# Performance work log

Hardware: AMD Instinct MI355X
Metric: run time of the kernel (lower is better)

The kernel has to match this reference:

```python
import jax, jax.numpy as jnp
import numpy as np

# --- constants from init_kwargs / module defaults ---
H, W, C = 720, 1280, 2
T_EVT, T_PROP = 10, 10
T_TOTAL = T_EVT + T_PROP          # 20 temporal steps (10 event + 10 propagation)
TAU, THR0 = 10.0, 1.0             # LIF time constant, base threshold
ALPHA, TARGET_RATE = 0.1, 0.1     # PENT adaptation
THR_MIN, THR_MAX = 0.1, 10.0
N_EVENTS = 4_000_000


def setup_inputs() -> dict:
    key = jax.random.key(0)
    k1, k2, k3, k4 = jax.random.split(key, 4)
    x = jax.random.randint(k1, (N_EVENTS,), 0, W, dtype=jnp.int32)
    y = jax.random.randint(k2, (N_EVENTS,), 0, H, dtype=jnp.int32)
    p = jax.random.randint(k3, (N_EVENTS,), 0, 2, dtype=jnp.int32)
    t = jax.random.uniform(k4, (N_EVENTS,), dtype=jnp.float32)
    return {"x": x, "y": y, "p": p, "t": t}


def _build_buffer(x, y, p, t):
    # TemporalBuffer.forward: bin events into first T_EVT steps, rest are zeros.
    tmin, tmax = t.min(), t.max()
    denom = jnp.where(tmax > tmin, tmax - tmin, jnp.float32(1.0))
    t_norm = jnp.where(tmax > tmin, (t - tmin) / denom * (T_EVT - 1e-6), 0.0)
    t_idx = jnp.clip(t_norm.astype(jnp.int32), 0, T_EVT - 1)
    xi = jnp.clip(x, 0, W - 1)
    yi = jnp.clip(y, 0, H - 1)
    c_idx = p  # p in {0,1} -> channel index directly (p.min() >= 0 branch)
    buf = jnp.zeros((T_TOTAL, C, H, W), jnp.float32)
    return buf.at[t_idx, c_idx, yi, xi].add(1.0)


def reference(x, y, p, t):
    buffer = _build_buffer(x, y, p, t)  # (T, C, H, W)
    decay = jnp.float32(np.exp(-1.0 / TAU))

    def step(carry, frame):
        mem, thr = carry
        # LIFBuffer: decay + accumulate
        mem = mem * decay + frame
        spk = (mem >= thr).astype(jnp.float32)
        mem = mem - spk * thr  # soft ('subtract') reset
        # AdaptiveThreshold (PENT): homeostatic rate-based adaptation
        rate = spk.mean()
        thr = jnp.clip(thr + ALPHA * (rate - TARGET_RATE), THR_MIN, THR_MAX)
        return (mem, thr), spk

    mem0 = jnp.zeros((C, H, W), jnp.float32)
    (_, _), spikes = jax.lax.scan(step, (mem0, jnp.float32(THR0)), buffer)
    return spikes  # (T, C, H, W) binary spike activity maps
```

## Files before the change

### kernel.cpp

```cpp
#include <hip/hip_runtime.h>
#include <cstddef>

#define HH 720
#define WW 1280
#define FRAME 1843200
#define FRAME4 460800
#define T_EVT 10
#define T_TOTAL 20
#define ARRIVE64 (1ULL << 32)

#define ONBLK 256
#define ONTHR 1024
#define ONWPB 16
#define ONT (ONBLK * ONTHR)

#define SBLK 1024
#define STHR 256
#define SWPB 4
#define PIXB 1800
#define NGROUP4 450
#define HIST_W 9000
#define RBLK 512
#define RTHR 1024
#define OTHR 512
#define NBUCKET 1024

#define MAT_OFF   0u
#define CS_OFF    (512u * 1024u * 4u)
#define SB_OFF    (CS_OFF + 4096u)
#define KEY_OFF   (SB_OFF + 8192u)
#define SEG_OFF(n) (KEY_OFF + 4u * (unsigned)(n))
#define WS_NEED(n) ((size_t)SEG_OFF(n) + 2ull * (size_t)(n) + 256ull)

__device__ unsigned g_minkey;
__device__ unsigned g_maxkey;
__device__ unsigned long long g_grp[T_TOTAL][16][16];
__device__ unsigned long long g_top[T_TOTAL][16];
__device__ unsigned g_rel[T_TOTAL][32];
__device__ unsigned long long g_n1[T_TOTAL][64][16];
__device__ unsigned long long g_n2[T_TOTAL][4][16];
__device__ unsigned long long g_n3[T_TOTAL][16];
__device__ unsigned g_relg[T_TOTAL][64][32];

__device__ __forceinline__ unsigned f2key(float f) {
    unsigned b = __float_as_uint(f);
    return b ^ ((unsigned)(((int)b) >> 31) | 0x80000000u);
}
__device__ __forceinline__ float key2f(unsigned k) {
    unsigned b = (k & 0x80000000u) ? (k ^ 0x80000000u) : ~k;
    return __uint_as_float(b);
}

__device__ __forceinline__ int event_bin_t(float tv, float tmin, float tmax) {
#pragma clang fp contract(off)
    float tn;
    if (tmax > tmin) tn = (tv - tmin) / (tmax - tmin) * (float)(10.0 - 1e-6);
    else tn = 0.0f;
    int ti = (int)tn;
    return ti < 0 ? 0 : (ti > T_EVT - 1 ? T_EVT - 1 : ti);
}
__device__ __forceinline__ int event_pixel(int xi, int yi, int ci) {
    xi = xi < 0 ? 0 : (xi > WW - 1 ? WW - 1 : xi);
    yi = yi < 0 ? 0 : (yi > HH - 1 ? HH - 1 : yi);
    return ci * (HH * WW) + yi * WW + xi;
}

__global__ void init_kernel() {
    const int gtid = blockIdx.x * blockDim.x + threadIdx.x;
    const int gs = gridDim.x * blockDim.x;
    if (gtid == 0) { g_minkey = 0xFFFFFFFFu; g_maxkey = 0u; }
    unsigned long long* a = &g_grp[0][0][0];
    for (int i = gtid; i < T_TOTAL * 16 * 16; i += gs) a[i] = 0ull;
    unsigned long long* b = &g_top[0][0];
    for (int i = gtid; i < T_TOTAL * 16; i += gs) b[i] = 0ull;
    unsigned* c = &g_rel[0][0];
    for (int i = gtid; i < T_TOTAL * 32; i += gs) c[i] = 0u;
    unsigned long long* d = &g_n1[0][0][0];
    for (int i = gtid; i < T_TOTAL * 64 * 16; i += gs) d[i] = 0ull;
    unsigned long long* e = &g_n2[0][0][0];
    for (int i = gtid; i < T_TOTAL * 4 * 16; i += gs) e[i] = 0ull;
    unsigned long long* f = &g_n3[0][0];
    for (int i = gtid; i < T_TOTAL * 16; i += gs) f[i] = 0ull;
    unsigned* g = &g_relg[0][0][0];
    for (int i = gtid; i < T_TOTAL * 64 * 32; i += gs) g[i] = 0u;
}

__device__ __forceinline__ void minmax_body(const float* __restrict__ t, int n,
                                            int gtid, int gstride) {
    unsigned mn = 0xFFFFFFFFu, mx = 0u;
    const int n4 = n >> 2;
    const float4* t4 = (const float4*)t;
    for (int i = gtid; i < n4; i += gstride) {
        float4 tv = t4[i];
        unsigned k0 = f2key(tv.x), k1 = f2key(tv.y);
        unsigned k2 = f2key(tv.z), k3 = f2key(tv.w);
        unsigned a = k0 < k1 ? k0 : k1, b = k2 < k3 ? k2 : k3;
        unsigned c = a < b ? a : b;
        mn = mn < c ? mn : c;
        a = k0 > k1 ? k0 : k1; b = k2 > k3 ? k2 : k3;
        c = a > b ? a : b;
        mx = mx > c ? mx : c;
    }
    for (int i = (n4 << 2) + gtid; i < n; i += gstride) {
        unsigned k = f2key(t[i]);
        mn = mn < k ? mn : k;
        mx = mx > k ? mx : k;
    }
    for (int off = 32; off > 0; off >>= 1) {
        unsigned omn = (unsigned)__shfl_down((int)mn, off, 64);
        unsigned omx = (unsigned)__shfl_down((int)mx, off, 64);
        mn = mn < omn ? mn : omn;
        mx = mx > omx ? mx : omx;
    }
    __shared__ unsigned smn[16], smx[16];
    int lane = threadIdx.x & 63, wv = threadIdx.x >> 6;
    if (lane == 0) { smn[wv] = mn; smx[wv] = mx; }
    __syncthreads();
    if (threadIdx.x == 0) {
        int nw = blockDim.x >> 6;
        for (int i = 1; i < nw; ++i) {
            mn = mn < smn[i] ? mn : smn[i];
            mx = mx > smx[i] ? mx : smx[i];
        }
        atomicMin(&g_minkey, mn);
        atomicMax(&g_maxkey, mx);
    }
}

__global__ void minmax_zero_kernel(const float* __restrict__ t, int n,
                                   uint4* __restrict__ hist16v) {
    const int gtid = blockIdx.x * blockDim.x + threadIdx.x;
    const int gstride = gridDim.x * blockDim.x;
    const uint4 z = make_uint4(0u, 0u, 0u, 0u);
    const int nz = T_EVT * FRAME / 8;
    for (int i = gtid; i < nz; i += gstride) hist16v[i] = z;
    minmax_body(t, n, gtid, gstride);
}

__global__ __launch_bounds__(RTHR) void passA_kernel(
        const int* __restrict__ x, const int* __restrict__ y,
        const int* __restrict__ p, const float* __restrict__ t,
        unsigned* __restrict__ mat, unsigned* __restrict__ keys, int n) {
    __shared__ unsigned cnt[NBUCKET];
    for (int i = threadIdx.x; i < NBUCKET; i += blockDim.x) cnt[i] = 0u;
    __syncthreads();
    const int chunk = (n + (int)gridDim.x - 1) / (int)gridDim.x;
    const int s0 = blockIdx.x * chunk;
    const int s1 = min(n, s0 + chunk);
    for (int i = s0 + threadIdx.x; i < s1; i += blockDim.x) {
        int pix = event_pixel(x[i], y[i], p[i]);
        keys[i] = (unsigned)pix;
        atomicAdd(&cnt[pix / PIXB], 1u);
    }
    minmax_body(t, n, blockIdx.x * blockDim.x + threadIdx.x,
                gridDim.x * blockDim.x);
    __syncthreads();
    for (int i = threadIdx.x; i < NBUCKET; i += blockDim.x)
        mat[blockIdx.x * NBUCKET + i] = cnt[i];
}

__global__ __launch_bounds__(OTHR) void offsets_col_kernel(
        unsigned* __restrict__ mat, unsigned* __restrict__ colsum) {
    const int j = blockIdx.x;
    const int r = threadIdx.x;
    const int lane = r & 63, wv = r >> 6;
    unsigned v = mat[r * NBUCKET + j];
    unsigned incl = v;
    for (int off = 1; off < 64; off <<= 1) {
        unsigned o = (unsigned)__shfl_up((int)incl, off, 64);
        if (lane >= off) incl += o;
    }
    __shared__ unsigned wtot[OTHR / 64];
    if (lane == 63) wtot[wv] = incl;
    __syncthreads();
    if (r == 0) {
        unsigned run = 0;
#pragma unroll
        for (int k = 0; k < OTHR / 64; ++k) { unsigned tmp = wtot[k]; wtot[k] = run; run += tmp; }
    }
    __syncthreads();
    unsigned ex = incl - v + wtot[wv];
    mat[r * NBUCKET + j] = ex;
    if (r == OTHR - 1) colsum[j] = ex + v;
}

__global__ __launch_bounds__(RTHR) void passB_kernel(
        const unsigned* __restrict__ keys, const float* __restrict__ t,
        const unsigned* __restrict__ mat, const unsigned* __restrict__ colsum,
        unsigned* __restrict__ seg_base_out,
        unsigned short* __restrict__ seg, int n) {
    __shared__ unsigned base[NBUCKET];
    __shared__ unsigned wt2[RTHR / 64];
    {
        const int j = threadIdx.x;
        const int lane = j & 63, wv = j >> 6;
        unsigned v = colsum[j];
        unsigned incl = v;
        for (int off = 1; off < 64; off <<= 1) {
            unsigned o = (unsigned)__shfl_up((int)incl, off, 64);
            if (lane >= off) incl += o;
        }
        if (lane == 63) wt2[wv] = incl;
        __syncthreads();
        if (j == 0) {
            unsigned run = 0;
#pragma unroll
            for (int k = 0; k < RTHR / 64; ++k) { unsigned tmp = wt2[k]; wt2[k] = run; run += tmp; }
        }
        __syncthreads();
        unsigned ex = incl - v + wt2[wv];
        base[j] = mat[blockIdx.x * NBUCKET + j] + ex;
        if (blockIdx.x == 0) {
            seg_base_out[j] = ex;
            if (j == NBUCKET - 1) seg_base_out[NBUCKET] = ex + v;
        }
    }
    __syncthreads();
    const float tmin = key2f(g_minkey);
    const float tmax = key2f(g_maxkey);
    const int chunk = (n + (int)gridDim.x - 1) / (int)gridDim.x;
    const int s0 = blockIdx.x * chunk;
    const int s1 = min(n, s0 + chunk);
    for (int i = s0 + threadIdx.x; i < s1; i += blockDim.x) {
        int pix = (int)keys[i];
        int ti = event_bin_t(t[i], tmin, tmax);
        int bkt = pix / PIXB;
        int lb = ti * PIXB + (pix - bkt * PIXB);
        unsigned idx = atomicAdd(&base[bkt], 1u);
        seg[idx] = (unsigned short)lb;
    }
}

__global__ __launch_bounds__(STHR, 4) void scan_new(float* __restrict__ out,
                                                    const unsigned short* __restrict__ seg,
                                                    const unsigned* __restrict__ seg_base) {
#pragma clang fp contract(off)
    const float decay = (float)0.9048374180359595;
    const int tid = threadIdx.x;
    const int lane = tid & 63;
    const int b = blockIdx.x;
    const int pix0 = b * PIXB;

    __shared__ unsigned lds_hist[HIST_W];
    __shared__ unsigned lds_arr[T_TOTAL];
    __shared__ unsigned lds_tot[T_TOTAL];

    for (int i = tid; i < HIST_W; i += STHR) lds_hist[i] = 0u;
    if (tid < T_TOTAL) { lds_arr[tid] = 0u; lds_tot[tid] = 0u; }
    __syncthreads();

    {
        const int e0 = (int)seg_base[b];
        const int e1 = (int)seg_base[b + 1];
        for (int i = e0 + tid; i < e1; i += STHR) {
            unsigned lb = seg[i];
            atomicAdd(&lds_hist[lb >> 1], 1u << ((lb & 1u) << 4));
        }
    }
    __syncthreads();

    const bool has1 = tid < (NGROUP4 - STHR);
    float4 mem0 = make_float4(0.f, 0.f, 0.f, 0.f);
    float4 mem1 = make_float4(0.f, 0.f, 0.f, 0.f);
    float thr = 1.0f;

    for (int s = 0; s < T_TOTAL; ++s) {
        float* ob = out + (size_t)s * FRAME + pix0;
        int cnt = 0;

        {
            float4 f;
            if (s < T_EVT) {
                int w = s * 900 + (tid << 1);
                unsigned w0 = lds_hist[w], w1 = lds_hist[w + 1];
                f = make_float4((float)(w0 & 0xFFFFu), (float)(w0 >> 16),
                                (float)(w1 & 0xFFFFu), (float)(w1 >> 16));
            } else f = make_float4(0.f, 0.f, 0.f, 0.f);
            float4 m, spk;
            m.x = mem0.x * decay; m.x = m.x + f.x;
            m.y = mem0.y * decay; m.y = m.y + f.y;
            m.z = mem0.z * decay; m.z = m.z + f.z;
            m.w = mem0.w * decay; m.w = m.w + f.w;
            spk.x = (m.x >= thr) ? 1.0f : 0.0f;
            spk.y = (m.y >= thr) ? 1.0f : 0.0f;
            spk.z = (m.z >= thr) ? 1.0f : 0.0f;
            spk.w = (m.w >= thr) ? 1.0f : 0.0f;
            ((float4*)ob)[tid] = spk;
            mem0.x = m.x - spk.x * thr;
            mem0.y = m.y - spk.y * thr;
            mem0.z = m.z - spk.z * thr;
            mem0.w = m.w - spk.w * thr;
            cnt += (int)spk.x + (int)spk.y + (int)spk.z + (int)spk.w;
        }
        if (has1) {
            int g = tid + STHR;
            float4 f;
            if (s < T_EVT) {
                int w = s * 900 + (g << 1);
                unsigned w0 = lds_hist[w], w1 = lds_hist[w + 1];
                f = make_float4((float)(w0 & 0xFFFFu), (float)(w0 >> 16),
                                (float)(w1 & 0xFFFFu), (float)(w1 >> 16));
            } else f = make_float4(0.f, 0.f, 0.f, 0.f);
            float4 m, spk;
            m.x = mem1.x * decay; m.x = m.x + f.x;
            m.y = mem1.y * decay; m.y = m.y + f.y;
            m.z = mem1.z * decay; m.z = m.z + f.z;
            m.w = mem1.w * decay; m.w = m.w + f.w;
            spk.x = (m.x >= thr) ? 1.0f : 0.0f;
            spk.y = (m.y >= thr) ? 1.0f : 0.0f;
            spk.z = (m.z >= thr) ? 1.0f : 0.0f;
            spk.w = (m.w >= thr) ? 1.0f : 0.0f;
            ((float4*)ob)[g] = spk;
            mem1.x = m.x - spk.x * thr;
            mem1.y = m.y - spk.y * thr;
            mem1.z = m.z - spk.z * thr;
            mem1.w = m.w - spk.w * thr;
            cnt += (int)spk.x + (int)spk.y + (int)spk.z + (int)spk.w;
        }

        if (s == T_TOTAL - 1) break;

        for (int off = 32; off > 0; off >>= 1) cnt += __shfl_down(cnt, off, 64);
        unsigned total;
        if (lane == 0) {
            unsigned old = __hip_atomic_fetch_add(&lds_arr[s],
                               (unsigned)cnt + (1u << 16),
                               __ATOMIC_RELAXED, __HIP_MEMORY_SCOPE_WORKGROUP);
            if ((old >> 16) == SWPB - 1) {
                unsigned bc = (old + (unsigned)cnt) & 0xFFFFu;
                const int g1 = b >> 4;
                unsigned long long a1 = __hip_atomic_fetch_add(
                    &g_n1[s][g1][0], (unsigned long long)bc + ARRIVE64,
                    __ATOMIC_RELAXED, __HIP_MEMORY_SCOPE_AGENT);
                if ((unsigned)(a1 >> 32) == 15u) {
                    unsigned c1 = (unsigned)a1 + bc;
                    const int g2 = g1 >> 4;
                    unsigned long long a2 = __hip_atomic_fetch_add(
                        &g_n2[s][g2][0], (unsigned long long)c1 + ARRIVE64,
                        __ATOMIC_RELAXED, __HIP_MEMORY_SCOPE_AGENT);
                    if ((unsigned)(a2 >> 32) == 15u) {
                        unsigned c2 = (unsigned)a2 + c1;
                        unsigned long long a3 = __hip_atomic_fetch_add(
                            &g_n3[s][0], (unsigned long long)c2 + ARRIVE64,
                            __ATOMIC_RELAXED, __HIP_MEMORY_SCOPE_AGENT);
                        if ((unsigned)(a3 >> 32) == 3u) {
                            unsigned tot = (unsigned)a3 + c2;
                            for (int g = 0; g < 64; ++g)
                                __hip_atomic_store(&g_relg[s][g][0], tot + 1u,
                                    __ATOMIC_RELAXED, __HIP_MEMORY_SCOPE_AGENT);
                        }
                    }
                }
                unsigned f;
                do {
                    __builtin_amdgcn_s_sleep(1);
                    f = __hip_atomic_load(&g_relg[s][g1][0], __ATOMIC_RELAXED,
                                          __HIP_MEMORY_SCOPE_AGENT);
                } while (f == 0u);
                total = f - 1u;
                __hip_atomic_store(&lds_tot[s], f,
                                   __ATOMIC_RELAXED, __HIP_MEMORY_SCOPE_WORKGROUP);
            } else {
                unsigned f;
                do {
                    __builtin_amdgcn_s_sleep(1);
                    f = __hip_atomic_load(&lds_tot[s], __ATOMIC_RELAXED,
                                          __HIP_MEMORY_SCOPE_WORKGROUP);
                } while (f == 0u);
                total = f - 1u;
            }
        }
        total = (unsigned)__shfl((int)total, 0, 64);
        float rate = (float)total / 1843200.0f;
        thr = thr + 0.1f * (rate - 0.1f);
        thr = fminf(fmaxf(thr, 0.1f), 10.0f);
    }
}

__global__ void scatter_kernel(const int* __restrict__ x, const int* __restrict__ y,
                               const int* __restrict__ p, const float* __restrict__ t,
                               unsigned* __restrict__ hist32, int n) {
    int i = blockIdx.x * blockDim.x + threadIdx.x;
    if (i >= n) return;
    float tmin = key2f(g_minkey);
    float tmax = key2f(g_maxkey);
    int ti = event_bin_t(t[i], tmin, tmax);
    int pix = event_pixel(x[i], y[i], p[i]);
    size_t bidx = (size_t)ti * FRAME + pix;
    atomicAdd(hist32 + (bidx >> 1), 1u << ((bidx & 1) << 4));
}

__global__ __launch_bounds__(ONTHR) void scan_old(float* __restrict__ out) {
#pragma clang fp contract(off)
    const float decay = (float)0.9048374180359595;
    const int gtid = blockIdx.x * ONTHR + threadIdx.x;
    const int lane = threadIdx.x & 63;
    const uint2 uz2 = make_uint2(0u, 0u);
    float4 mem0 = make_float4(0.f, 0.f, 0.f, 0.f);
    float4 mem1 = make_float4(0.f, 0.f, 0.f, 0.f);
    const bool has1 = (gtid + ONT) < FRAME4;
    float thr = 1.0f;
    const uint2* hist2 = (const uint2*)(out + (size_t)T_EVT * FRAME);
    __shared__ unsigned lds_arr[T_TOTAL];
    __shared__ unsigned lds_tot[T_TOTAL];
    if (threadIdx.x < T_TOTAL) { lds_arr[threadIdx.x] = 0u; lds_tot[threadIdx.x] = 0u; }
    __syncthreads();
    uint2 u0 = hist2[gtid];
    uint2 u1 = has1 ? hist2[gtid + ONT] : uz2;
    for (int s = 0; s < T_TOTAL; ++s) {
        float4* o4 = (float4*)(out + (size_t)s * FRAME);
        int cnt = 0;
        {
            float4 m, spk;
            m.x = mem0.x * decay; m.x = m.x + (float)(u0.x & 0xFFFFu);
            m.y = mem0.y * decay; m.y = m.y + (float)(u0.x >> 16);
            m.z = mem0.z * decay; m.z = m.z + (float)(u0.y & 0xFFFFu);
            m.w = mem0.w * decay; m.w = m.w + (float)(u0.y >> 16);
            spk.x = (m.x >= thr) ? 1.0f : 0.0f;
            spk.y = (m.y >= thr) ? 1.0f : 0.0f;
            spk.z = (m.z >= thr) ? 1.0f : 0.0f;
            spk.w = (m.w >= thr) ? 1.0f : 0.0f;
            o4[gtid] = spk;
            mem0.x = m.x - spk.x * thr; mem0.y = m.y - spk.y * thr;
            mem0.z = m.z - spk.z * thr; mem0.w = m.w - spk.w * thr;
            cnt += (int)spk.x + (int)spk.y + (int)spk.z + (int)spk.w;
        }
        if (has1) {
            float4 m, spk;
            m.x = mem1.x * decay; m.x = m.x + (float)(u1.x & 0xFFFFu);
            m.y = mem1.y * decay; m.y = m.y + (float)(u1.x >> 16);
            m.z = mem1.z * decay; m.z = m.z + (float)(u1.y & 0xFFFFu);
            m.w = mem1.w * decay; m.w = m.w + (float)(u1.y >> 16);
            spk.x = (m.x >= thr) ? 1.0f : 0.0f;
            spk.y = (m.y >= thr) ? 1.0f : 0.0f;
            spk.z = (m.z >= thr) ? 1.0f : 0.0f;
            spk.w = (m.w >= thr) ? 1.0f : 0.0f;
            o4[gtid + ONT] = spk;
            mem1.x = m.x - spk.x * thr; mem1.y = m.y - spk.y * thr;
            mem1.z = m.z - spk.z * thr; mem1.w = m.w - spk.w * thr;
            cnt += (int)spk.x + (int)spk.y + (int)spk.z + (int)spk.w;
        }
        if (s + 1 < T_EVT) {
            const uint2* hn = hist2 + (size_t)(s + 1) * FRAME4;
            u0 = hn[gtid];
            u1 = has1 ? hn[gtid + ONT] : uz2;
        } else { u0 = uz2; u1 = uz2; }
        if (s == T_TOTAL - 1) break;
        for (int off = 32; off > 0; off >>= 1) cnt += __shfl_down(cnt, off, 64);
        unsigned total;
        if (lane == 0) {
            unsigned old = __hip_atomic_fetch_add(&lds_arr[s],
                               (unsigned)cnt + (1u << 16),
                               __ATOMIC_RELAXED, __HIP_MEMORY_SCOPE_WORKGROUP);
            if ((old >> 16) == ONWPB - 1) {
                unsigned bc = (old + (unsigned)cnt) & 0xFFFFu;
                const int gid = blockIdx.x >> 4;
                unsigned long long gold = __hip_atomic_fetch_add(
                    &g_grp[s][gid][0], (unsigned long long)bc + ARRIVE64,
                    __ATOMIC_RELAXED, __HIP_MEMORY_SCOPE_AGENT);
                if ((unsigned)(gold >> 32) == 15u) {
                    unsigned gc = (unsigned)gold + bc;
                    unsigned long long told = __hip_atomic_fetch_add(
                        &g_top[s][0], (unsigned long long)gc + ARRIVE64,
                        __ATOMIC_RELAXED, __HIP_MEMORY_SCOPE_AGENT);
                    if ((unsigned)(told >> 32) == 15u) {
                        unsigned tot = (unsigned)told + gc;
                        __hip_atomic_store(&g_rel[s][0], tot + 1u,
                                           __ATOMIC_RELAXED, __HIP_MEMORY_SCOPE_AGENT);
                    }
                }
                unsigned f;
                do {
                    __builtin_amdgcn_s_sleep(1);
                    f = __hip_atomic_load(&g_rel[s][0], __ATOMIC_RELAXED,
                                          __HIP_MEMORY_SCOPE_AGENT);
                } while (f == 0u);
                total = f - 1u;
                __hip_atomic_store(&lds_tot[s], f,
                                   __ATOMIC_RELAXED, __HIP_MEMORY_SCOPE_WORKGROUP);
            } else {
                unsigned f;
                do {
                    __builtin_amdgcn_s_sleep(1);
                    f = __hip_atomic_load(&lds_tot[s], __ATOMIC_RELAXED,
                                          __HIP_MEMORY_SCOPE_WORKGROUP);
                } while (f == 0u);
                total = f - 1u;
            }
        }
        total = (unsigned)__shfl((int)total, 0, 64);
        float rate = (float)total / 1843200.0f;
        thr = thr + 0.1f * (rate - 0.1f);
        thr = fminf(fmaxf(thr, 0.1f), 10.0f);
    }
}

extern "C" void kernel_launch(void* const* d_in, const int* in_sizes, int n_in,
                              void* d_out, int out_size, void* d_ws, size_t ws_size,
                              hipStream_t stream) {
    const int*   x = (const int*)d_in[0];
    const int*   y = (const int*)d_in[1];
    const int*   p = (const int*)d_in[2];
    const float* t = (const float*)d_in[3];
    float* out = (float*)d_out;
    const int n = in_sizes[0];

    init_kernel<<<64, 256, 0, stream>>>();

    if (d_ws != nullptr && ws_size >= WS_NEED(n)) {
        unsigned* mat = (unsigned*)((char*)d_ws + MAT_OFF);
        unsigned* colsum = (unsigned*)((char*)d_ws + CS_OFF);
        unsigned* seg_base = (unsigned*)((char*)d_ws + SB_OFF);
        unsigned* keys = (unsigned*)((char*)d_ws + KEY_OFF);
        unsigned short* seg = (unsigned short*)((char*)d_ws + SEG_OFF(n));

        passA_kernel<<<RBLK, RTHR, 0, stream>>>(x, y, p, t, mat, keys, n);
        offsets_col_kernel<<<NBUCKET, OTHR, 0, stream>>>(mat, colsum);
        passB_kernel<<<RBLK, RTHR, 0, stream>>>(keys, t, mat, colsum, seg_base, seg, n);

        dim3 g(SBLK), b(STHR);
        void* args[] = { (void*)&out, (void*)&seg, (void*)&seg_base };
        hipLaunchCooperativeKernel((void*)scan_new, g, b, args, 0, stream);
    } else {
        unsigned* hist32 = (unsigned*)(out + (size_t)T_EVT * FRAME);
        minmax_zero_kernel<<<1024, 256, 0, stream>>>(t, n, (uint4*)hist32);
        scatter_kernel<<<(n + 255) / 256, 256, 0, stream>>>(x, y, p, t, hist32, n);
        dim3 g(ONBLK), b(ONTHR);
        void* args[] = { (void*)&out };
        hipLaunchCooperativeKernel((void*)scan_old, g, b, args, 0, stream);
    }
}
```

Baseline: 350.9 us.

## Drop init kernel, use per-block minmax partials, overlap next-frame load with barrier

Removes the separate init kernel launch on the workspace path by zeroing the hierarchical-barrier counters inside passA. Global min/max atomics are replaced by per-block partial results that offsets_col reduces in one block. In the scan kernel, the next frame's histogram load and the membrane decay are moved between the barrier arrival and the spin-wait, so that work overlaps the cross-block synchronisation. The risk is that in the workspace path the g_grp/g_top/g_rel counters are no longer reset, which matters only if some path still uses them.

```diff
diff --git a/kernel.cpp b/kernel.cpp
--- a/kernel.cpp
+++ b/kernel.cpp
@@ -34,6 +34,8 @@
 
 __device__ unsigned g_minkey;
 __device__ unsigned g_maxkey;
+__device__ unsigned g_part_mn[RBLK];
+__device__ unsigned g_part_mx[RBLK];
 __device__ unsigned long long g_grp[T_TOTAL][16][16];
 __device__ unsigned long long g_top[T_TOTAL][16];
 __device__ unsigned g_rel[T_TOTAL][32];
@@ -75,14 +77,6 @@
     for (int i = gtid; i < T_TOTAL * 16; i += gs) b[i] = 0ull;
     unsigned* c = &g_rel[0][0];
     for (int i = gtid; i < T_TOTAL * 32; i += gs) c[i] = 0u;
-    unsigned long long* d = &g_n1[0][0][0];
-    for (int i = gtid; i < T_TOTAL * 64 * 16; i += gs) d[i] = 0ull;
-    unsigned long long* e = &g_n2[0][0][0];
-    for (int i = gtid; i < T_TOTAL * 4 * 16; i += gs) e[i] = 0ull;
-    unsigned long long* f = &g_n3[0][0];
-    for (int i = gtid; i < T_TOTAL * 16; i += gs) f[i] = 0ull;
-    unsigned* g = &g_relg[0][0][0];
-    for (int i = gtid; i < T_TOTAL * 64 * 32; i += gs) g[i] = 0u;
 }
 
 __device__ __forceinline__ void minmax_body(const float* __restrict__ t, int n,
@@ -127,6 +121,48 @@
     }
 }
 
+__device__ __forceinline__ void minmax_part_body(const float* __restrict__ t, int n,
+                                                 int gtid, int gstride) {
+    unsigned mn = 0xFFFFFFFFu, mx = 0u;
+    const int n4 = n >> 2;
+    const float4* t4 = (const float4*)t;
+    for (int i = gtid; i < n4; i += gstride) {
+        float4 tv = t4[i];
+        unsigned k0 = f2key(tv.x), k1 = f2key(tv.y);
+        unsigned k2 = f2key(tv.z), k3 = f2key(tv.w);
+        unsigned a = k0 < k1 ? k0 : k1, b = k2 < k3 ? k2 : k3;
+        unsigned c = a < b ? a : b;
+        mn = mn < c ? mn : c;
+        a = k0 > k1 ? k0 : k1; b = k2 > k3 ? k2 : k3;
+        c = a > b ? a : b;
+        mx = mx > c ? mx : c;
+    }
+    for (int i = (n4 << 2) + gtid; i < n; i += gstride) {
+        unsigned k = f2key(t[i]);
+        mn = mn < k ? mn : k;
+        mx = mx > k ? mx : k;
+    }
+    for (int off = 32; off > 0; off >>= 1) {
+        unsigned omn = (unsigned)__shfl_down((int)mn, off, 64);
+        unsigned omx = (unsigned)__shfl_down((int)mx, off, 64);
+        mn = mn < omn ? mn : omn;
+        mx = mx > omx ? mx : omx;
+    }
+    __shared__ unsigned smn[16], smx[16];
+    int lane = threadIdx.x & 63, wv = threadIdx.x >> 6;
+    if (lane == 0) { smn[wv] = mn; smx[wv] = mx; }
+    __syncthreads();
+    if (threadIdx.x == 0) {
+        int nw = blockDim.x >> 6;
+        for (int i = 1; i < nw; ++i) {
+            mn = mn < smn[i] ? mn : smn[i];
+            mx = mx > smx[i] ? mx : smx[i];
+        }
+        g_part_mn[blockIdx.x] = mn;
+        g_part_mx[blockIdx.x] = mx;
+    }
+}
+
 __global__ void minmax_zero_kernel(const float* __restrict__ t, int n,
                                    uint4* __restrict__ hist16v) {
     const int gtid = blockIdx.x * blockDim.x + threadIdx.x;
@@ -142,6 +178,18 @@
         const int* __restrict__ p, const float* __restrict__ t,
         unsigned* __restrict__ mat, unsigned* __restrict__ keys, int n) {
     __shared__ unsigned cnt[NBUCKET];
+    const int gtid = blockIdx.x * blockDim.x + threadIdx.x;
+    const int gs = gridDim.x * blockDim.x;
+    {
+        unsigned long long* z1 = &g_n1[0][0][0];
+        for (int i = gtid; i < T_TOTAL * 64 * 16; i += gs) z1[i] = 0ull;
+        unsigned long long* z2 = &g_n2[0][0][0];
+        for (int i = gtid; i < T_TOTAL * 4 * 16; i += gs) z2[i] = 0ull;
+        unsigned long long* z3 = &g_n3[0][0];
+        for (int i = gtid; i < T_TOTAL * 16; i += gs) z3[i] = 0ull;
+        unsigned* z4 = &g_relg[0][0][0];
+        for (int i = gtid; i < T_TOTAL * 64 * 32; i += gs) z4[i] = 0u;
+    }
     for (int i = threadIdx.x; i < NBUCKET; i += blockDim.x) cnt[i] = 0u;
     __syncthreads();
     const int chunk = (n + (int)gridDim.x - 1) / (int)gridDim.x;
@@ -152,8 +200,7 @@
         keys[i] = (unsigned)pix;
         atomicAdd(&cnt[pix / PIXB], 1u);
     }
-    minmax_body(t, n, blockIdx.x * blockDim.x + threadIdx.x,
-                gridDim.x * blockDim.x);
+    minmax_part_body(t, n, gtid, gs);
     __syncthreads();
     for (int i = threadIdx.x; i < NBUCKET; i += blockDim.x)
         mat[blockIdx.x * NBUCKET + i] = cnt[i];
@@ -182,6 +229,28 @@
     unsigned ex = incl - v + wtot[wv];
     mat[r * NBUCKET + j] = ex;
     if (r == OTHR - 1) colsum[j] = ex + v;
+
+    if (j == 0) {
+        unsigned mn = g_part_mn[r], mx = g_part_mx[r];
+        for (int off = 32; off > 0; off >>= 1) {
+            unsigned omn = (unsigned)__shfl_down((int)mn, off, 64);
+            unsigned omx = (unsigned)__shfl_down((int)mx, off, 64);
+            mn = mn < omn ? mn : omn;
+            mx = mx > omx ? mx : omx;
+        }
+        __shared__ unsigned smn2[OTHR / 64], smx2[OTHR / 64];
+        if (lane == 0) { smn2[wv] = mn; smx2[wv] = mx; }
+        __syncthreads();
+        if (r == 0) {
+#pragma unroll
+            for (int k = 1; k < OTHR / 64; ++k) {
+                mn = mn < smn2[k] ? mn : smn2[k];
+                mx = mx > smx2[k] ? mx : smx2[k];
+            }
+            g_minkey = mn;
+            g_maxkey = mx;
+        }
+    }
 }
 
 __global__ __launch_bounds__(RTHR) void passB_kernel(
@@ -241,7 +310,7 @@
     const int b = blockIdx.x;
     const int pix0 = b * PIXB;
 
-    __shared__ unsigned lds_hist[HIST_W];
+    __shared__ alignas(16) unsigned lds_hist[HIST_W];
     __shared__ unsigned lds_arr[T_TOTAL];
     __shared__ unsigned lds_tot[T_TOTAL];
 
@@ -264,23 +333,28 @@
     float4 mem1 = make_float4(0.f, 0.f, 0.f, 0.f);
     float thr = 1.0f;
 
-    for (int s = 0; s < T_TOTAL; ++s) {
+    float4 f0, f1;
+    {
+        uint2 w01 = *(const uint2*)&lds_hist[tid << 1];
+        f0 = make_float4((float)(w01.x & 0xFFFFu), (float)(w01.x >> 16),
+                         (float)(w01.y & 0xFFFFu), (float)(w01.y >> 16));
+        if (has1) {
+            uint2 v = *(const uint2*)&lds_hist[(tid + STHR) << 1];
+            f1 = make_float4((float)(v.x & 0xFFFFu), (float)(v.x >> 16),
+                             (float)(v.y & 0xFFFFu), (float)(v.y >> 16));
+        } else f1 = make_float4(0.f, 0.f, 0.f, 0.f);
+    }
+
+    for (int s = 0;; ++s) {
         float* ob = out + (size_t)s * FRAME + pix0;
         int cnt = 0;
 
         {
-            float4 f;
-            if (s < T_EVT) {
-                int w = s * 900 + (tid << 1);
-                unsigned w0 = lds_hist[w], w1 = lds_hist[w + 1];
-                f = make_float4((float)(w0 & 0xFFFFu), (float)(w0 >> 16),
-                                (float)(w1 & 0xFFFFu), (float)(w1 >> 16));
-            } else f = make_float4(0.f, 0.f, 0.f, 0.f);
             float4 m, spk;
-            m.x = mem0.x * decay; m.x = m.x + f.x;
-            m.y = mem0.y * decay; m.y = m.y + f.y;
-            m.z = mem0.z * decay; m.z = m.z + f.z;
-            m.w = mem0.w * decay; m.w = m.w + f.w;
+            m.x = mem0.x + f0.x;
+            m.y = mem0.y + f0.y;
+            m.z = mem0.z + f0.z;
+            m.w = mem0.w + f0.w;
             spk.x = (m.x >= thr) ? 1.0f : 0.0f;
             spk.y = (m.y >= thr) ? 1.0f : 0.0f;
             spk.z = (m.z >= thr) ? 1.0f : 0.0f;
@@ -294,18 +368,11 @@
         }
         if (has1) {
             int g = tid + STHR;
-            float4 f;
-            if (s < T_EVT) {
-                int w = s * 900 + (g << 1);
-                unsigned w0 = lds_hist[w], w1 = lds_hist[w + 1];
-                f = make_float4((float)(w0 & 0xFFFFu), (float)(w0 >> 16),
-                                (float)(w1 & 0xFFFFu), (float)(w1 >> 16));
-            } else f = make_float4(0.f, 0.f, 0.f, 0.f);
             float4 m, spk;
-            m.x = mem1.x * decay; m.x = m.x + f.x;
-            m.y = mem1.y * decay; m.y = m.y + f.y;
-            m.z = mem1.z * decay; m.z = m.z + f.z;
-            m.w = mem1.w * decay; m.w = m.w + f.w;
+            m.x = mem1.x + f1.x;
+            m.y = mem1.y + f1.y;
+            m.z = mem1.z + f1.z;
+            m.w = mem1.w + f1.w;
             spk.x = (m.x >= thr) ? 1.0f : 0.0f;
             spk.y = (m.y >= thr) ? 1.0f : 0.0f;
             spk.z = (m.z >= thr) ? 1.0f : 0.0f;
@@ -321,14 +388,16 @@
         if (s == T_TOTAL - 1) break;
 
         for (int off = 32; off > 0; off >>= 1) cnt += __shfl_down(cnt, off, 64);
-        unsigned total;
+
+        bool last = false;
+        const int g1 = b >> 4;
         if (lane == 0) {
             unsigned old = __hip_atomic_fetch_add(&lds_arr[s],
                                (unsigned)cnt + (1u << 16),
                                __ATOMIC_RELAXED, __HIP_MEMORY_SCOPE_WORKGROUP);
             if ((old >> 16) == SWPB - 1) {
+                last = true;
                 unsigned bc = (old + (unsigned)cnt) & 0xFFFFu;
-                const int g1 = b >> 4;
                 unsigned long long a1 = __hip_atomic_fetch_add(
                     &g_n1[s][g1][0], (unsigned long long)bc + ARRIVE64,
                     __ATOMIC_RELAXED, __HIP_MEMORY_SCOPE_AGENT);
@@ -351,7 +420,35 @@
                         }
                     }
                 }
-                unsigned f;
+            }
+        }
+
+        {
+            const int sn = s + 1;
+            if (sn < T_EVT) {
+                uint2 w01 = *(const uint2*)&lds_hist[sn * 900 + (tid << 1)];
+                f0 = make_float4((float)(w01.x & 0xFFFFu), (float)(w01.x >> 16),
+                                 (float)(w01.y & 0xFFFFu), (float)(w01.y >> 16));
+                if (has1) {
+                    uint2 v = *(const uint2*)&lds_hist[sn * 900 + ((tid + STHR) << 1)];
+                    f1 = make_float4((float)(v.x & 0xFFFFu), (float)(v.x >> 16),
+                                     (float)(v.y & 0xFFFFu), (float)(v.y >> 16));
+                }
+            } else {
+                f0 = make_float4(0.f, 0.f, 0.f, 0.f);
+                f1 = make_float4(0.f, 0.f, 0.f, 0.f);
+            }
+            mem0.x = mem0.x * decay; mem0.y = mem0.y * decay;
+            mem0.z = mem0.z * decay; mem0.w = mem0.w * decay;
+            mem1.x = mem1.x * decay; mem1.y = mem1.y * decay;
+            mem1.z = mem1.z * decay; mem1.w = mem1.w * decay;
+        }
+        __builtin_amdgcn_sched_barrier(0);
+
+        unsigned total = 0u;
+        if (lane == 0) {
+            unsigned f;
+            if (last) {
                 do {
                     __builtin_amdgcn_s_sleep(1);
                     f = __hip_atomic_load(&g_relg[s][g1][0], __ATOMIC_RELAXED,
@@ -361,13 +458,13 @@
                 __hip_atomic_store(&lds_tot[s], f,
                                    __ATOMIC_RELAXED, __HIP_MEMORY_SCOPE_WORKGROUP);
             } else {
-                unsigned f;
+                unsigned f2;
                 do {
                     __builtin_amdgcn_s_sleep(1);
-                    f = __hip_atomic_load(&lds_tot[s], __ATOMIC_RELAXED,
-                                          __HIP_MEMORY_SCOPE_WORKGROUP);
-                } while (f == 0u);
-                total = f - 1u;
+                    f2 = __hip_atomic_load(&lds_tot[s], __ATOMIC_RELAXED,
+                                           __HIP_MEMORY_SCOPE_WORKGROUP);
+                } while (f2 == 0u);
+                total = f2 - 1u;
             }
         }
         total = (unsigned)__shfl((int)total, 0, 64);
@@ -447,7 +544,7 @@
         } else { u0 = uz2; u1 = uz2; }
         if (s == T_TOTAL - 1) break;
         for (int off = 32; off > 0; off >>= 1) cnt += __shfl_down(cnt, off, 64);
-        unsigned total;
+        unsigned total = 0u;
         if (lane == 0) {
             unsigned old = __hip_atomic_fetch_add(&lds_arr[s],
                                (unsigned)cnt + (1u << 16),
@@ -505,8 +602,6 @@
     float* out = (float*)d_out;
     const int n = in_sizes[0];
 
-    init_kernel<<<64, 256, 0, stream>>>();
-
     if (d_ws != nullptr && ws_size >= WS_NEED(n)) {
         unsigned* mat = (unsigned*)((char*)d_ws + MAT_OFF);
         unsigned* colsum = (unsigned*)((char*)d_ws + CS_OFF);
@@ -522,6 +617,7 @@
         void* args[] = { (void*)&out, (void*)&seg, (void*)&seg_base };
         hipLaunchCooperativeKernel((void*)scan_new, g, b, args, 0, stream);
     } else {
+        init_kernel<<<64, 256, 0, stream>>>();
         unsigned* hist32 = (unsigned*)(out + (size_t)T_EVT * FRAME);
         minmax_zero_kernel<<<1024, 256, 0, stream>>>(t, n, (uint4*)hist32);
         scatter_kernel<<<(n + 255) / 256, 256, 0, stream>>>(x, y, p, t, hist32, n);
```

New measurement: 344.9 us. About the same (-1.7%).
